# Kernel optimization log

Measured on AMD Instinct MI355X. Metric: run time of the kernel, lower is better.

Reference implementation:

```python
import jax, jax.numpy as jnp
import numpy as np
from jax.scipy.special import logsumexp

B, T, LD, HD, K = 64, 2048, 16, 64, 8
TEMP = 1.0  # annealing=False
LOG2PI = float(np.log(2.0 * np.pi))


def setup_inputs() -> dict:
    key = jax.random.key(0)
    ks = jax.random.split(key, 10)
    return {
        "z": jax.random.normal(ks[0], (B, T, LD), jnp.float32),
        "pi": jax.random.normal(ks[1], (K,), jnp.float32) * 0.5,
        "Q": jax.random.normal(ks[2], (K, K), jnp.float32) * 0.5,
        "init_mean": jax.random.normal(ks[3], (K, LD), jnp.float32),
        # torch init: rand(K,1,1) * eye(LD) * 5  (a scale factor per state)
        "init_cov": jax.random.uniform(ks[4], (K, 1, 1), jnp.float32) * 5.0 * jnp.eye(LD, dtype=jnp.float32)[None],
        "covs": jnp.tile(jnp.eye(LD, dtype=jnp.float32)[None], (K, 1, 1)) + 0.05 * jax.random.normal(ks[5], (K, LD, LD), jnp.float32),
        "W1": jax.random.normal(ks[6], (K, HD, LD), jnp.float32) / np.sqrt(LD),
        "b1": jnp.zeros((K, HD), jnp.float32),
        "W2": jax.random.normal(ks[7], (K, LD, HD), jnp.float32) / np.sqrt(HD),
        "b2": jnp.zeros((K, LD), jnp.float32),
    }


def _chol_terms(C):
    """Sigma = C C^T + 1e-6 I ; return (L^{-1}, 0.5*logdet) per state."""
    dim = C.shape[-1]
    Sigma = C @ jnp.swapaxes(C, -1, -2) + 1e-6 * jnp.eye(dim, dtype=C.dtype)
    L = jnp.linalg.cholesky(Sigma)  # [K,D,D]
    Linv = jax.vmap(lambda l: jax.scipy.linalg.solve_triangular(l, jnp.eye(dim, dtype=C.dtype), lower=True))(L)
    logdet_half = jnp.sum(jnp.log(jnp.diagonal(L, axis1=-2, axis2=-1)), -1)  # [K]
    return Linv, logdet_half


def _mvn_logp(diff, Linv, logdet_half):
    # diff [B,t,K,D], Linv [K,D,D] -> [B,t,K]
    y = jnp.einsum('kde,btke->btkd', Linv, diff)
    maha = jnp.sum(y * y, -1)
    d = diff.shape[-1]
    return -0.5 * maha - logdet_half - 0.5 * d * LOG2PI


def reference(z, pi, Q, init_mean, init_cov, covs, W1, b1, W2, b2):
    # ---- local evidence: log p(z_1|s_1), log p(z_t | z_{t-1}, s_t)  [B,T,K]
    Linv0, ld0 = _chol_terms(init_cov)
    le1 = _mvn_logp(z[:, :1, None, :] - init_mean, Linv0, ld0)  # [B,1,K]
    zp = z[:, :-1]  # [B,T-1,D]
    h = jax.nn.softplus(jnp.einsum('btd,khd->btkh', zp, W1) + b1)  # per-state MLP hidden
    mu = jnp.einsum('btkh,kdh->btkd', h, W2) + b2  # [B,T-1,K,D]
    LinvT, ldT = _chol_terms(covs)
    leT = _mvn_logp(z[:, 1:, None, :] - mu, LinvT, ldT)  # [B,T-1,K]
    le = jnp.concatenate([le1, leT], axis=1)  # [B,T,K]

    # ---- alpha recursion (filtering)
    logpi = jax.nn.log_softmax(pi / TEMP)
    Qlog = jax.nn.log_softmax(Q / TEMP, axis=-1)  # log p(s_t=j | s_{t-1}=i)
    QT = Qlog.T  # [to, from]
    lp0 = le[:, 0] + logpi
    lz0 = logsumexp(lp0, -1)
    la0 = lp0 - lz0[:, None]
    le_rest = jnp.swapaxes(le[:, 1:], 0, 1)  # [T-1,B,K]

    def astep(la_prev, le_t):
        lp = logsumexp(le_t[:, :, None] + QT[None] + la_prev[:, None, :], axis=-1)
        lz = logsumexp(lp, -1)
        la = lp - lz[:, None]
        return la, (la, lz)

    _, (las, lzs) = jax.lax.scan(astep, la0, le_rest)
    log_alpha = jnp.concatenate([la0[:, None], jnp.swapaxes(las, 0, 1)], axis=1)  # [B,T,K]
    log_Z = jnp.concatenate([lz0[:, None], lzs.T], axis=1)  # [B,T]

    # ---- beta recursion (smoothing), reverse scan
    def bstep(lb_next, inp):
        le_t, lz_t = inp
        lb = logsumexp(Qlog[None] + le_t[:, None, :] + lb_next[:, None, :], axis=-1) - lz_t[:, None]
        return lb, lb

    _, lbs = jax.lax.scan(bstep, jnp.zeros((B, K), le.dtype), (le_rest, log_Z[:, 1:].T), reverse=True)
    log_beta = jnp.concatenate([jnp.swapaxes(lbs, 0, 1), jnp.zeros((B, 1, K), le.dtype)], axis=1)

    # ---- posteriors
    gamma = jnp.exp(log_alpha + log_beta)  # [B,T,K]
    paired = jnp.exp(Qlog[None, None] + log_alpha[:, :-1, :, None] + log_beta[:, 1:, None, :] + le[:, 1:, None, :] - log_Z[:, 1:, None, None])  # [B,T-1,K,K]
    return gamma, paired, log_Z
```

## Files before the change

kernel.cpp:

```cpp
#include <hip/hip_runtime.h>

#define B_ 64
#define T_ 2048
#define LD_ 16
#define HD_ 64
#define K_ 8
#define L_ 16
#define C_ 128
#define S_ 16

constexpr int OFF_LE    = 0;
constexpr int OFF_ALPHA = 1048576;
constexpr int OFF_EBAR  = 2097152;
constexpr int OFF_ZT    = OFF_ALPHA;
constexpr int OFF_PBUF  = 3145728;
constexpr int OFF_RLOG  = 3670016;
constexpr int OFF_SBUF  = 3809280;
constexpr int OFF_UBUF  = 3874816;
constexpr int OFF_ULOG  = 3940352;
constexpr int OFF_SAIN  = 3941376;
constexpr int OFF_BENT  = 3949568;
constexpr int OFF_PRM   = 3957760;

constexpr int P_LINV0 = 0;
constexpr int P_LINVT = 2048;
constexpr int P_LD0   = 4096;
constexpr int P_LDT   = 4104;
constexpr int P_LOGPI = 4112;
constexpr int P_QEXP  = 4120;
constexpr int P_QTEXP = 4184;

constexpr int FI_NC2 = 32768;
constexpr int FI_C0I = 32896;

constexpr int OUT_PAIRED = B_*T_*K_;
constexpr int OUT_LOGZ   = OUT_PAIRED + B_*(T_-1)*K_*K_;

template<int CTRL>
__device__ __forceinline__ float dppmov(float x) {
  int xi = __float_as_int(x);
  int r = __builtin_amdgcn_update_dpp(xi, xi, CTRL, 0xF, 0xF, true);
  return __int_as_float(r);
}
__device__ __forceinline__ void allg8(float v, float w[8]) {
  w[0] = v;
  w[1] = dppmov<0xB1>(v);
  w[2] = dppmov<0x4E>(v);
  w[3] = dppmov<0x4E>(w[1]);
  w[7] = dppmov<0x141>(v);
  w[6] = dppmov<0xB1>(w[7]);
  w[5] = dppmov<0x4E>(w[7]);
  w[4] = dppmov<0x4E>(w[6]);
}
template<int V> __device__ __forceinline__ float xorg8(float x);
template<> __device__ __forceinline__ float xorg8<0>(float x) { return x; }
template<> __device__ __forceinline__ float xorg8<1>(float x) { return dppmov<0xB1>(x); }
template<> __device__ __forceinline__ float xorg8<2>(float x) { return dppmov<0x4E>(x); }
template<> __device__ __forceinline__ float xorg8<3>(float x) { return dppmov<0x4E>(dppmov<0xB1>(x)); }
template<> __device__ __forceinline__ float xorg8<4>(float x) { return dppmov<0x4E>(dppmov<0xB1>(dppmov<0x141>(x))); }
template<> __device__ __forceinline__ float xorg8<5>(float x) { return dppmov<0x4E>(dppmov<0x141>(x)); }
template<> __device__ __forceinline__ float xorg8<6>(float x) { return dppmov<0xB1>(dppmov<0x141>(x)); }
template<> __device__ __forceinline__ float xorg8<7>(float x) { return dppmov<0x141>(x); }

__device__ __forceinline__ float bfly_sum8(float x) {
  x += dppmov<0xB1>(x); x += dppmov<0x4E>(x); x += dppmov<0x141>(x); return x;
}
__device__ __forceinline__ float bfly_max8(float x) {
  x = fmaxf(x, dppmov<0xB1>(x)); x = fmaxf(x, dppmov<0x4E>(x)); x = fmaxf(x, dppmov<0x141>(x)); return x;
}
__device__ __forceinline__ float rcpnr(float x) {
  float r0 = __builtin_amdgcn_rcpf(x);
  return r0 * __builtin_fmaf(-x, r0, 2.0f);
}
__device__ __forceinline__ void absg8(float v, float w[8]) {
  int x = __float_as_int(v);
  w[0] = __int_as_float(__builtin_amdgcn_ds_swizzle(x, 0x18));
  w[1] = __int_as_float(__builtin_amdgcn_ds_swizzle(x, 0x38));
  w[2] = __int_as_float(__builtin_amdgcn_ds_swizzle(x, 0x58));
  w[3] = __int_as_float(__builtin_amdgcn_ds_swizzle(x, 0x78));
  w[4] = __int_as_float(__builtin_amdgcn_ds_swizzle(x, 0x98));
  w[5] = __int_as_float(__builtin_amdgcn_ds_swizzle(x, 0xB8));
  w[6] = __int_as_float(__builtin_amdgcn_ds_swizzle(x, 0xD8));
  w[7] = __int_as_float(__builtin_amdgcn_ds_swizzle(x, 0xF8));
}
__device__ __forceinline__ void col2row(const float cl[8], float rv[8]) {
  rv[0] = cl[0];
  rv[1] = xorg8<1>(cl[1]);
  rv[2] = xorg8<2>(cl[2]);
  rv[3] = xorg8<3>(cl[3]);
  rv[4] = xorg8<4>(cl[4]);
  rv[5] = xorg8<5>(cl[5]);
  rv[6] = xorg8<6>(cl[6]);
  rv[7] = xorg8<7>(cl[7]);
}
__device__ __forceinline__ void mmul8(const float a[8], const float m[8], float o[8]) {
  float m8[8][8];
  #pragma unroll
  for (int w = 0; w < 8; w++) allg8(m[w], m8[w]);
  #pragma unroll
  for (int v = 0; v < 8; v++) {
    float acc = 0.f;
    #pragma unroll
    for (int u = 0; u < 8; u++) acc = __builtin_fmaf(a[u], m8[u^v][u], acc);
    o[v] = acc;
  }
}
__device__ __forceinline__ float maxnorm8(float m[8]) {
  float mx = m[0];
  #pragma unroll
  for (int u = 1; u < 8; u++) mx = fmaxf(mx, m[u]);
  mx = bfly_max8(mx);
  float r = rcpnr(mx);
  #pragma unroll
  for (int u = 0; u < 8; u++) m[u] *= r;
  return mx;
}
__device__ __forceinline__ void load_rows(const float* p, float r[8]) {
  const float4* q = (const float4*)p;
  float4 x0 = q[0], x1 = q[1];
  r[0]=x0.x; r[1]=x0.y; r[2]=x0.z; r[3]=x0.w;
  r[4]=x1.x; r[5]=x1.y; r[6]=x1.z; r[7]=x1.w;
}
__device__ __forceinline__ float dotw8(const float r[8], const float w[8]) {
  return ((r[0]*w[0]+r[1]*w[1]) + (r[2]*w[2]+r[3]*w[3]))
       + ((r[4]*w[4]+r[5]*w[5]) + (r[6]*w[6]+r[7]*w[7]));
}

typedef __attribute__((ext_vector_type(4))) float f32x4;
typedef __attribute__((ext_vector_type(8))) short bf16x8;

__device__ __forceinline__ unsigned ph(float a, float b) {
  return (__float_as_uint(a) >> 16) | (__float_as_uint(b) & 0xFFFF0000u);
}
__device__ __forceinline__ float hif(float a) {
  return __uint_as_float(__float_as_uint(a) & 0xFFFF0000u);
}
__device__ __forceinline__ bf16x8 u2f(uint4 u) {
  return __builtin_bit_cast(bf16x8, u);
}
__device__ __forceinline__ bf16x8 mkfrag(float4 v) {
  unsigned ux = __float_as_uint(v.x), uy = __float_as_uint(v.y);
  unsigned uz = __float_as_uint(v.z), uw = __float_as_uint(v.w);
  unsigned h01 = (ux >> 16) | (uy & 0xFFFF0000u);
  unsigned h23 = (uz >> 16) | (uw & 0xFFFF0000u);
  float lx = v.x - __uint_as_float(ux & 0xFFFF0000u);
  float ly = v.y - __uint_as_float(uy & 0xFFFF0000u);
  float lz = v.z - __uint_as_float(uz & 0xFFFF0000u);
  float lw = v.w - __uint_as_float(uw & 0xFFFF0000u);
  unsigned l01 = ph(lx, ly);
  unsigned l23 = ph(lz, lw);
  return u2f(make_uint4(h01, h23, l01, l23));
}
__device__ __forceinline__ f32x4 MF(bf16x8 a, bf16x8 b, f32x4 c) {
  return __builtin_amdgcn_mfma_f32_16x16x32_bf16(a, b, c, 0, 0, 0);
}

__global__ __launch_bounds__(64) void prep_kernel(
    const float* __restrict__ pi, const float* __restrict__ Q,
    const float* __restrict__ init_cov, const float* __restrict__ covs,
    float* __restrict__ prm)
{
  int tid = threadIdx.x;
  int blk = blockIdx.x;
  if (blk < 16) {
    int k = blk & 7;
    const float* C = (blk < 8 ? init_cov : covs) + k*256;
    float* outL  = prm + (blk < 8 ? P_LINV0 : P_LINVT) + k*256;
    float* outld = prm + (blk < 8 ? P_LD0   : P_LDT)   + k;
    __shared__ float S[16][17], L[16][17], X[16][17];
    for (int e = tid; e < 256; e += 64) {
      int r = e >> 4, c = e & 15;
      float s = (r == c) ? 1e-6f : 0.f;
      for (int l = 0; l < 16; l++) s += C[r*16+l] * C[c*16+l];
      S[r][c] = s;
    }
    __syncthreads();
    for (int j = 0; j < 16; j++) {
      if (tid == 0) L[j][j] = sqrtf(S[j][j]);
      __syncthreads();
      if (tid > j && tid < 16) L[tid][j] = S[tid][j] / L[j][j];
      __syncthreads();
      if (tid > j && tid < 16) {
        float ltj = L[tid][j];
        for (int c = j+1; c <= tid; c++) S[tid][c] -= ltj * L[c][j];
      }
      __syncthreads();
    }
    if (tid < 16) {
      int c = tid;
      for (int r = 0; r < 16; r++) {
        float v;
        if (r < c) v = 0.f;
        else {
          v = (r == c) ? 1.f : 0.f;
          for (int s2 = c; s2 < r; s2++) v -= L[r][s2] * X[s2][c];
          v /= L[r][r];
        }
        X[r][c] = v;
      }
    }
    __syncthreads();
    for (int e = tid; e < 256; e += 64) outL[e] = X[e>>4][e&15];
    if (tid == 0) {
      float ld = 0.f;
      for (int j = 0; j < 16; j++) ld += logf(L[j][j]);
      *outld = ld;
    }
  } else {
    if (tid < 8) {
      int row = tid;
      float q[8], mx = -1e30f;
      for (int j = 0; j < 8; j++) { q[j] = Q[row*8+j]; mx = fmaxf(mx, q[j]); }
      float s = 0.f;
      for (int j = 0; j < 8; j++) s += __expf(q[j]-mx);
      float ls = logf(s);
      for (int j = 0; j < 8; j++) {
        float e = __expf(q[j]-mx-ls);
        prm[P_QEXP  + row*8 + j] = e;
        prm[P_QTEXP + j*8 + row] = e;
      }
    } else if (tid == 8) {
      float p[8], mx = -1e30f;
      for (int j = 0; j < 8; j++) { p[j] = pi[j]; mx = fmaxf(mx, p[j]); }
      float s = 0.f;
      for (int j = 0; j < 8; j++) s += __expf(p[j]-mx);
      float ls = logf(s);
      for (int j = 0; j < 8; j++) prm[P_LOGPI+j] = p[j]-mx-ls;
    }
  }
}

__global__ __launch_bounds__(64) void prep2_kernel(
    const float* __restrict__ W1, const float* __restrict__ W2,
    const float* __restrict__ b2, const float* __restrict__ init_mean,
    const float* __restrict__ prm, float* __restrict__ frag)
{
  int k = blockIdx.x, tid = threadIdx.x;
  __shared__ float Ls[16][16], L0s[16][16], G[16][64];
  for (int e = tid; e < 256; e += 64) {
    Ls[e>>4][e&15]  = prm[P_LINVT + k*256 + e];
    L0s[e>>4][e&15] = prm[P_LINV0 + k*256 + e];
  }
  __syncthreads();
  for (int idx = tid; idx < 1024; idx += 64) {
    int d = idx >> 6, hh = idx & 63;
    float s = 0.f;
    for (int e = 0; e < 16; e++) s += Ls[d][e] * W2[k*1024 + e*64 + hh];
    G[d][hh] = -s;
  }
  __syncthreads();
  int d = tid & 15, q = tid >> 4;
  uint4* F4 = (uint4*)frag;
  for (int kc = 0; kc < 2; kc++) {
    float v[8], lo[8];
    for (int j = 0; j < 8; j++) {
      int hh = 32*kc + 16*(j>>2) + 4*q + (j&3);
      v[j] = G[d][hh];
      lo[j] = v[j] - hif(v[j]);
    }
    F4[6144 + ((k*2+kc)*4+q)*16 + d] =
        make_uint4(ph(v[0],v[1]), ph(v[2],v[3]), ph(v[4],v[5]), ph(v[6],v[7]));
    F4[7168 + ((k*2+kc)*4+q)*16 + d] =
        make_uint4(ph(lo[0],lo[1]), ph(lo[2],lo[3]), ph(lo[4],lo[5]), ph(lo[6],lo[7]));
  }
  for (int mt = 0; mt < 4; mt++) {
    int hh = 16*mt + d;
    float v[4], lo[4];
    for (int j = 0; j < 4; j++) { v[j] = W1[k*1024 + hh*16 + 4*q + j]; lo[j] = v[j] - hif(v[j]); }
    unsigned x = ph(v[0],v[1]), y = ph(v[2],v[3]);
    F4[((k*4+mt)*4+q)*16 + d]        = make_uint4(x, y, x, y);
    F4[2048 + ((k*4+mt)*4+q)*16 + d] = make_uint4(ph(lo[0],lo[1]), ph(lo[2],lo[3]), 0u, 0u);
  }
  {
    float v[4], lo[4];
    for (int j = 0; j < 4; j++) { v[j] = Ls[d][4*q+j]; lo[j] = v[j] - hif(v[j]); }
    unsigned x = ph(v[0],v[1]), y = ph(v[2],v[3]);
    F4[4096 + (k*4+q)*16 + d] = make_uint4(x, y, x, y);
    F4[4608 + (k*4+q)*16 + d] = make_uint4(ph(lo[0],lo[1]), ph(lo[2],lo[3]), 0u, 0u);
    for (int j = 0; j < 4; j++) { v[j] = L0s[d][4*q+j]; lo[j] = v[j] - hif(v[j]); }
    x = ph(v[0],v[1]); y = ph(v[2],v[3]);
    F4[5120 + (k*4+q)*16 + d] = make_uint4(x, y, x, y);
    F4[5632 + (k*4+q)*16 + d] = make_uint4(ph(lo[0],lo[1]), ph(lo[2],lo[3]), 0u, 0u);
  }
  if (q == 0) {
    float s2 = 0.f, s0 = 0.f;
    for (int e = 0; e < 16; e++) {
      s2 += Ls[d][e]  * b2[k*16+e];
      s0 += L0s[d][e] * init_mean[k*16+e];
    }
    frag[FI_NC2 + k*16 + d] = -s2;
    frag[FI_C0I + k*16 + d] = -s0;
  }
}

__global__ __launch_bounds__(256) void ztr_kernel(
    const float* __restrict__ z, float* __restrict__ zt)
{
  int tid = blockIdx.x*256 + threadIdx.x;
  int t = tid >> 6, b = tid & 63;
  const float4* src = (const float4*)(z + (b*T_ + t)*LD_);
  float4* dst = (float4*)(zt + t*1024 + b*16);
  dst[0] = src[0]; dst[1] = src[1]; dst[2] = src[2]; dst[3] = src[3];
}

__global__ __launch_bounds__(256) void emisB_kernel(
    const float* __restrict__ zt, const float* __restrict__ b1,
    const float* __restrict__ frag, const float* __restrict__ prm,
    float* __restrict__ lebuf)
{
  int lane = threadIdx.x & 63;
  int wid = __builtin_amdgcn_readfirstlane(blockIdx.x*4 + (threadIdx.x >> 6));
  int bblk = wid & 3;
  int tch  = (wid >> 2) & 255;
  int k    = wid >> 10;
  int c = lane & 15, q = lane >> 4;
  int b = bblk*16 + c;
  const uint4* F4 = (const uint4*)frag;

  bf16x8 w1a1[4], w1a2[4];
  #pragma unroll
  for (int mt = 0; mt < 4; mt++) {
    w1a1[mt] = u2f(F4[((k*4+mt)*4+q)*16 + c]);
    w1a2[mt] = u2f(F4[2048 + ((k*4+mt)*4+q)*16 + c]);
  }
  bf16x8 lva1 = u2f(F4[4096 + (k*4+q)*16 + c]);
  bf16x8 lva2 = u2f(F4[4608 + (k*4+q)*16 + c]);
  bf16x8 gahi[2], galo[2];
  #pragma unroll
  for (int kc = 0; kc < 2; kc++) {
    gahi[kc] = u2f(F4[6144 + ((k*2+kc)*4+q)*16 + c]);
    galo[kc] = u2f(F4[7168 + ((k*2+kc)*4+q)*16 + c]);
  }
  float b1iv[16];
  #pragma unroll
  for (int i = 0; i < 16; i++)
    b1iv[i] = b1[k*64 + (i>>2)*16 + 4*q + (i&3)];
  float nc2[4];
  #pragma unroll
  for (int r = 0; r < 4; r++) nc2[r] = frag[FI_NC2 + k*16 + 4*q + r];
  float lconst = -prm[P_LDT + k] - 14.70301653f;

  int t0 = tch*8;
  bf16x8 zp;
  int ttstart;
  if (tch == 0) {
    float4 zv0 = *(const float4*)(zt + b*16 + 4*q);
    bf16x8 zc0 = mkfrag(zv0);
    bf16x8 l0a1 = u2f(F4[5120 + (k*4+q)*16 + c]);
    bf16x8 l0a2 = u2f(F4[5632 + (k*4+q)*16 + c]);
    f32x4 acc;
    acc[0] = frag[FI_C0I + k*16 + 4*q + 0];
    acc[1] = frag[FI_C0I + k*16 + 4*q + 1];
    acc[2] = frag[FI_C0I + k*16 + 4*q + 2];
    acc[3] = frag[FI_C0I + k*16 + 4*q + 3];
    acc = MF(l0a1, zc0, acc);
    acc = MF(l0a2, zc0, acc);
    float m2 = (acc[0]*acc[0] + acc[1]*acc[1]) + (acc[2]*acc[2] + acc[3]*acc[3]);
    m2 += __shfl_xor(m2, 16);
    m2 += __shfl_xor(m2, 32);
    float le = -0.5f*m2 - prm[P_LD0+k] - 14.70301653f + prm[P_LOGPI+k];
    if (q == 0) lebuf[k*64 + b] = le;
    zp = zc0;
    ttstart = 1;
  } else {
    float4 zvp = *(const float4*)(zt + (t0-1)*1024 + b*16 + 4*q);
    zp = mkfrag(zvp);
    ttstart = 0;
  }

  float4 zv = *(const float4*)(zt + (t0+ttstart)*1024 + b*16 + 4*q);
  #pragma unroll 1
  for (int tt = ttstart; tt < 8; tt++) {
    int t = t0 + tt;
    float4 zvn = zv;
    if (tt < 7) zvn = *(const float4*)(zt + (t+1)*1024 + b*16 + 4*q);
    bf16x8 zc = mkfrag(zv);
    f32x4 a1[4];
    #pragma unroll
    for (int mt = 0; mt < 4; mt++) {
      f32x4 ai;
      ai[0] = b1iv[mt*4+0]; ai[1] = b1iv[mt*4+1];
      ai[2] = b1iv[mt*4+2]; ai[3] = b1iv[mt*4+3];
      ai = MF(w1a1[mt], zp, ai);
      a1[mt] = MF(w1a2[mt], zp, ai);
    }
    float hv[16];
    #pragma unroll
    for (int i = 0; i < 16; i++) {
      float a = a1[i>>2][i&3];
      hv[i] = fmaxf(a, 0.f) + __logf(1.f + __expf(-fabsf(a)));
    }
    bf16x8 hhi[2], hlo[2];
    #pragma unroll
    for (int kc = 0; kc < 2; kc++) {
      const float* hp = hv + 8*kc;
      hhi[kc] = u2f(make_uint4(ph(hp[0],hp[1]), ph(hp[2],hp[3]),
                               ph(hp[4],hp[5]), ph(hp[6],hp[7])));
      float l0 = hp[0]-hif(hp[0]), l1 = hp[1]-hif(hp[1]);
      float l2 = hp[2]-hif(hp[2]), l3 = hp[3]-hif(hp[3]);
      float l4 = hp[4]-hif(hp[4]), l5 = hp[5]-hif(hp[5]);
      float l6 = hp[6]-hif(hp[6]), l7 = hp[7]-hif(hp[7]);
      hlo[kc] = u2f(make_uint4(ph(l0,l1), ph(l2,l3), ph(l4,l5), ph(l6,l7)));
    }
    f32x4 acc;
    acc[0] = nc2[0]; acc[1] = nc2[1]; acc[2] = nc2[2]; acc[3] = nc2[3];
    acc = MF(lva1, zc, acc);
    acc = MF(lva2, zc, acc);
    #pragma unroll
    for (int kc = 0; kc < 2; kc++) {
      acc = MF(gahi[kc], hhi[kc], acc);
      acc = MF(galo[kc], hhi[kc], acc);
      acc = MF(gahi[kc], hlo[kc], acc);
    }
    float m2 = (acc[0]*acc[0] + acc[1]*acc[1]) + (acc[2]*acc[2] + acc[3]*acc[3]);
    m2 += __shfl_xor(m2, 16);
    m2 += __shfl_xor(m2, 32);
    float le = -0.5f*m2 + lconst;
    if (q == 0) lebuf[t*512 + k*64 + b] = le;
    zp = zc;
    zv = zvn;
  }
}

__global__ __launch_bounds__(256) void fwdA_kernel(
    const float* __restrict__ lebuf, const float* __restrict__ prm,
    float* __restrict__ pbuf, float* __restrict__ sbuf)
{
  int lane64 = threadIdx.x & 63;
  int iu = threadIdx.x >> 6;
  int unit = blockIdx.x*4 + iu;
  int b = unit & 63, s = unit >> 6;
  int u = lane64 >> 3, j = lane64 & 7;
  int c = 8*s + u;
  float qtv[64];
  #pragma unroll
  for (int x = 0; x < 8; x++)
    #pragma unroll
    for (int v = 0; v < 8; v++)
      qtv[x*8+v] = prm[P_QTEXP + (j^x)*8 + (j^v)];
  float lev[16];
  #pragma unroll
  for (int x = 0; x < 16; x++) lev[x] = lebuf[(c*L_+x)*512 + j*64 + b];
  float pl[8];
  if (c == 0) {
    float m = bfly_max8(lev[0]);
    float e = __expf(lev[0]-m);
    allg8(e, pl);
  } else {
    float m = bfly_max8(lev[0]);
    float e = __expf(lev[0]-m);
    float e8[8]; allg8(e, e8);
    float np[8];
    #pragma unroll
    for (int x = 0; x < 8; x++) np[x] = e8[x] * qtv[x*8];
    float mx = np[0];
    #pragma unroll
    for (int x = 1; x < 8; x++) mx = fmaxf(mx, np[x]);
    mx = bfly_max8(mx);
    float r = rcpnr(mx);
    #pragma unroll
    for (int x = 0; x < 8; x++) pl[x] = np[x] * r;
  }
  #pragma unroll
  for (int sx = 1; sx < 16; sx++) {
    float m = bfly_max8(lev[sx]);
    float e = __expf(lev[sx]-m);
    float e8[8]; allg8(e, e8);
    float np[8];
    #pragma unroll
    for (int x = 0; x < 8; x++) {
      float acc = 0.f;
      #pragma unroll
      for (int v = 0; v < 8; v++) acc = __builtin_fmaf(qtv[x*8+v], pl[v], acc);
      np[x] = e8[x] * acc;
    }
    float mx = np[0];
    #pragma unroll
    for (int x = 1; x < 8; x++) mx = fmaxf(mx, np[x]);
    mx = bfly_max8(mx);
    float r = rcpnr(mx);
    #pragma unroll
    for (int x = 0; x < 8; x++) pl[x] = np[x] * r;
  }
  float rv[8]; col2row(pl, rv);
  float4* dst = (float4*)(pbuf + (c*64 + b)*64 + j*8);
  dst[0] = make_float4(rv[0], rv[1], rv[2], rv[3]);
  dst[1] = make_float4(rv[4], rv[5], rv[6], rv[7]);
  __shared__ float M[4][8][64];
  #pragma unroll
  for (int v = 0; v < 8; v++) M[iu][u][j*8+v] = rv[v];
  __syncthreads();
  if (u == 0) {
    float m[8];
    #pragma unroll
    for (int v = 0; v < 8; v++) m[v] = M[iu][0][j*8+v];
    for (int cc = 1; cc < 8; cc++) {
      float a[8];
      #pragma unroll
      for (int v = 0; v < 8; v++) a[v] = M[iu][cc][j*8+v];
      float nm[8];
      mmul8(a, m, nm);
      maxnorm8(nm);
      #pragma unroll
      for (int v = 0; v < 8; v++) m[v] = nm[v];
    }
    float4* d2 = (float4*)(sbuf + (s*64 + b)*64 + j*8);
    d2[0] = make_float4(m[0], m[1], m[2], m[3]);
    d2[1] = make_float4(m[4], m[5], m[6], m[7]);
  }
}

__global__ __launch_bounds__(512) void fwdP2b_kernel(
    const float* __restrict__ sbuf, float* __restrict__ sain)
{
  int lane = threadIdx.x;
  int b = lane >> 3, i = lane & 7;
  const float4* base = (const float4*)sbuf;
  float4 c0 = base[(0*64+b)*16 + i*2], c1 = base[(0*64+b)*16 + i*2 + 1];
  float a = 0.125f;
  for (int s = 0; s < 16; s++) {
    int s2 = (s < 15) ? s+1 : 15;
    float4 n0 = base[(s2*64+b)*16 + i*2], n1 = base[(s2*64+b)*16 + i*2 + 1];
    float aw[8]; allg8(a, aw);
    float sm = ((c0.x*aw[0] + c0.y*aw[1]) + (c0.z*aw[2] + c0.w*aw[3]))
             + ((c1.x*aw[4] + c1.y*aw[5]) + (c1.z*aw[6] + c1.w*aw[7]));
    float tot = bfly_sum8(sm);
    float an = sm * rcpnr(tot);
    if (s < 15) { a = an; sain[(s+1)*512 + b*8 + i] = a; }
    c0 = n0; c1 = n1;
  }
}

__global__ __launch_bounds__(256) void fwdB_kernel(
    const float* __restrict__ lebuf, const float* __restrict__ prm,
    const float* __restrict__ sain, float* pbuf,
    float* __restrict__ alpha, float* __restrict__ ebar,
    float* __restrict__ rlog, float* __restrict__ ubuf,
    float* __restrict__ ulog, float* __restrict__ out)
{
  int lane64 = threadIdx.x & 63;
  int iu = threadIdx.x >> 6;
  int unit = blockIdx.x*4 + iu;
  int b = unit & 63, s = unit >> 6;
  int u = lane64 >> 3, i = lane64 & 7;
  int c = 8*s + u;
  int off = b*8 + i;
  __shared__ float Als[4][8];
  __shared__ float Mh[4][8][64];
  __shared__ float Lh[4][8];
  float pr[8];
  load_rows(pbuf + (c*64 + b)*64 + i*8, pr);
  float lev[16];
  #pragma unroll
  for (int x = 0; x < 16; x++) lev[x] = lebuf[(c*L_+x)*512 + i*64 + b];
  float av_in = 0.f;
  if (u == 0) av_in = (s == 0) ? 0.125f : sain[s*512 + off];
  for (int r = 0; r < 7; r++) {
    if (u == r) {
      if (r > 0) av_in = Als[iu][i];
      float aw[8]; allg8(av_in, aw);
      float sm = dotw8(pr, aw);
      float tot = bfly_sum8(sm);
      Als[iu][i] = sm * rcpnr(tot);
    }
    __syncthreads();
  }
  if (u == 7) av_in = Als[iu][i];
  float q[8];
  #pragma unroll
  for (int x = 0; x < 8; x++) q[x] = prm[P_QTEXP + i*8 + (i^x)];
  float* logZ = out + OUT_LOGZ + b*T_;
  float eb_loc[16];
  float a;
  if (c == 0) {
    float m0 = bfly_max8(lev[0]);
    float e0x = __expf(lev[0]-m0);
    float ct = bfly_sum8(e0x);
    float rr = rcpnr(ct);
    a = e0x * rr;
    alpha[off] = a;
    eb_loc[0] = a;
    ebar[off] = a;
    if (i == 0) logZ[0] = m0 + __logf(ct);
  } else {
    a = av_in;
    int t = c*L_;
    float m = bfly_max8(lev[0]);
    float e = __expf(lev[0]-m);
    float w[8]; allg8(a, w);
    float dot = dotw8(q, w);
    float p = e * dot;
    float ct = bfly_sum8(p);
    float rr = rcpnr(ct);
    a = p * rr;
    alpha[t*512 + off] = a;
    float eb = e * rr;
    eb_loc[0] = eb;
    ebar[t*512 + off] = eb;
    if (i == 0) logZ[t] = m + __logf(ct);
  }
  #pragma unroll
  for (int x = 1; x < 16; x++) {
    int t = c*L_ + x;
    float m = bfly_max8(lev[x]);
    float e = __expf(lev[x]-m);
    float w[8]; allg8(a, w);
    float dot = dotw8(q, w);
    float p = e * dot;
    float ct = bfly_sum8(p);
    float rr = rcpnr(ct);
    a = p * rr;
    alpha[t*512 + off] = a;
    float eb = e * rr;
    eb_loc[x] = eb;
    ebar[t*512 + off] = eb;
    if (i == 0) logZ[t] = m + __logf(ct);
  }
  float qv[64];
  #pragma unroll
  for (int x = 0; x < 8; x++)
    #pragma unroll
    for (int v = 0; v < 8; v++)
      qv[x*8+v] = prm[P_QEXP + (i^x)*8 + (i^v)];
  float rl8[8];
  #pragma unroll
  for (int x = 0; x < 8; x++) rl8[x] = (x == 0) ? 1.f : 0.f;
  float lsc = 0.f;
  #pragma unroll
  for (int sx = 15; sx >= 1; sx--) {
    float e8[8]; allg8(eb_loc[sx], e8);
    float nr[8];
    #pragma unroll
    for (int x = 0; x < 8; x++) {
      float acc = 0.f;
      #pragma unroll
      for (int v = 0; v < 8; v++) acc = __builtin_fmaf(qv[x*8+v], e8[v]*rl8[v], acc);
      nr[x] = acc;
    }
    float mx = nr[0];
    #pragma unroll
    for (int x = 1; x < 8; x++) mx = fmaxf(mx, nr[x]);
    mx = bfly_max8(mx);
    float r = rcpnr(mx);
    #pragma unroll
    for (int x = 0; x < 8; x++) rl8[x] = nr[x] * r;
    lsc += __logf(mx);
  }
  float rv[8]; col2row(rl8, rv);
  float4* dstR = (float4*)(pbuf + (c*64 + b)*64 + i*8);
  dstR[0] = make_float4(rv[0], rv[1], rv[2], rv[3]);
  dstR[1] = make_float4(rv[4], rv[5], rv[6], rv[7]);
  if (i == 0) rlog[c*64 + b] = lsc;
  float qr[8];
  #pragma unroll
  for (int x = 0; x < 8; x++) qr[x] = prm[P_QEXP + i*8 + (i^x)];
  float d8[8];
  #pragma unroll
  for (int v = 0; v < 8; v++) d8[v] = eb_loc[0] * rv[v];
  float h8[8];
  mmul8(qr, d8, h8);
  float ls = lsc + __logf(maxnorm8(h8));
  #pragma unroll
  for (int v = 0; v < 8; v++) Mh[iu][u][i*8+v] = h8[v];
  if (i == 0) Lh[iu][u] = ls;
  __syncthreads();
  if (u == 0) {
    float m[8];
    #pragma unroll
    for (int v = 0; v < 8; v++) m[v] = Mh[iu][7][i*8+v];
    float lsum = Lh[iu][7];
    for (int cc = 6; cc >= 0; cc--) {
      float aa[8];
      #pragma unroll
      for (int v = 0; v < 8; v++) aa[v] = Mh[iu][cc][i*8+v];
      float t8[8];
      mmul8(aa, m, t8);
      lsum += Lh[iu][cc] + __logf(maxnorm8(t8));
      #pragma unroll
      for (int v = 0; v < 8; v++) m[v] = t8[v];
    }
    float4* d2 = (float4*)(ubuf + (s*64 + b)*64 + i*8);
    d2[0] = make_float4(m[0], m[1], m[2], m[3]);
    d2[1] = make_float4(m[4], m[5], m[6], m[7]);
    if (i == 0) ulog[s*64 + b] = lsum;
  }
}

__global__ __launch_bounds__(512) void bwdP2b_kernel(
    const float* __restrict__ ubuf, const float* __restrict__ ulog,
    float* __restrict__ bent)
{
  int lane = threadIdx.x;
  int b = lane >> 3, i = lane & 7;
  bent[15*512 + b*8 + i] = 1.f;
  const float4* base = (const float4*)ubuf;
  float sh = 1.f, sig = 0.f;
  float4 c0 = base[(15*64+b)*16 + i*2], c1 = base[(15*64+b)*16 + i*2 + 1];
  float cu = ulog[15*64 + b];
  for (int s = 15; s >= 1; s--) {
    int s2 = (s > 1) ? s-1 : 1;
    float4 n0 = base[(s2*64+b)*16 + i*2], n1 = base[(s2*64+b)*16 + i*2 + 1];
    float nu = ulog[s2*64 + b];
    float sw[8]; allg8(sh, sw);
    float y = ((c0.x*sw[0] + c0.y*sw[1]) + (c0.z*sw[2] + c0.w*sw[3]))
            + ((c1.x*sw[4] + c1.y*sw[5]) + (c1.z*sw[6] + c1.w*sw[7]));
    float mx = bfly_max8(y);
    sh = y * rcpnr(mx);
    sig += cu + __logf(mx);
    bent[(s-1)*512 + b*8 + i] = sh * __expf(sig);
    c0 = n0; c1 = n1; cu = nu;
  }
}

__global__ __launch_bounds__(256) void bwdC_kernel(
    const float* __restrict__ alpha, const float* __restrict__ ebar,
    const float* __restrict__ rbuf, const float* __restrict__ rlog,
    const float* __restrict__ prm, const float* __restrict__ bent,
    float* __restrict__ out)
{
  int lane64 = threadIdx.x & 63;
  int iu = threadIdx.x >> 6;
  int unit = blockIdx.x*4 + iu;
  int b = unit & 63, s = unit >> 6;
  int u = lane64 >> 3, i = lane64 & 7;
  int c = 8*s + u;
  int off = b*8 + i;
  float qr[8], qa[8];
  #pragma unroll
  for (int x = 0; x < 8; x++) qr[x] = prm[P_QEXP + i*8 + (i^x)];
  #pragma unroll
  for (int v = 0; v < 8; v++) qa[v] = prm[P_QEXP + i*8 + v];
  float r8[8];
  load_rows(rbuf + (c*64 + b)*64 + i*8, r8);
  float e0 = ebar[(c*L_)*512 + off];
  float erl = __expf(rlog[c*64 + b]);
  float av[16], ev[16];
  #pragma unroll
  for (int x = 0; x < 16; x++) av[x] = alpha[(c*L_+x)*512 + off];
  #pragma unroll
  for (int x = 1; x < 16; x++) ev[x] = ebar[(c*L_+x)*512 + off];
  float avm1 = (c > 0) ? alpha[(c*L_-1)*512 + off] : 0.f;
  __shared__ float Bls[4][8];
  float bt = 0.f, y = 0.f, nbv = 0.f;
  for (int r = 7; r >= 0; r--) {
    if (u == r) {
      bt = (r == 7) ? bent[s*512 + off] : Bls[iu][i];
      float bw[8]; allg8(bt, bw);
      y = dotw8(r8, bw) * erl;
      float ey = e0 * y;
      float w[8]; allg8(ey, w);
      nbv = 0.f;
      #pragma unroll
      for (int v = 0; v < 8; v++) nbv = __builtin_fmaf(qr[v], w[v], nbv);
      if (r > 0) Bls[iu][i] = nbv;
    }
    __syncthreads();
  }
  float* po = out + OUT_PAIRED + b*((T_-1)*64);
  float* go = out + b*(T_*K_);
  float bb = bt;
  if (c == 127) go[2047*8 + i] = av[15];
  #pragma unroll
  for (int x = 15; x >= 1; x--) {
    float eya[8]; absg8(ev[x]*bb, eya);
    float term[8];
    #pragma unroll
    for (int v = 0; v < 8; v++) term[v] = qa[v]*eya[v];
    float nb = ((term[0]+term[1]) + (term[2]+term[3]))
             + ((term[4]+term[5]) + (term[6]+term[7]));
    int t = c*L_ + x - 1;
    float am = av[x-1];
    float4* pd = (float4*)(po + t*64 + i*8);
    pd[0] = make_float4(am*term[0], am*term[1], am*term[2], am*term[3]);
    pd[1] = make_float4(am*term[4], am*term[5], am*term[6], am*term[7]);
    go[t*8 + i] = am*nb;
    bb = nb;
  }
  if (c > 0) {
    float eya[8]; absg8(e0*y, eya);
    int t = c*L_ - 1;
    float4* pd = (float4*)(po + t*64 + i*8);
    pd[0] = make_float4(avm1*qa[0]*eya[0], avm1*qa[1]*eya[1],
                        avm1*qa[2]*eya[2], avm1*qa[3]*eya[3]);
    pd[1] = make_float4(avm1*qa[4]*eya[4], avm1*qa[5]*eya[5],
                        avm1*qa[6]*eya[6], avm1*qa[7]*eya[7]);
    go[t*8 + i] = avm1 * nbv;
  }
}

extern "C" void kernel_launch(void* const* d_in, const int* in_sizes, int n_in,
                              void* d_out, int out_size, void* d_ws, size_t ws_size,
                              hipStream_t stream) {
  const float* z         = (const float*)d_in[0];
  const float* pi        = (const float*)d_in[1];
  const float* Q         = (const float*)d_in[2];
  const float* init_mean = (const float*)d_in[3];
  const float* init_cov  = (const float*)d_in[4];
  const float* covs      = (const float*)d_in[5];
  const float* W1        = (const float*)d_in[6];
  const float* b1        = (const float*)d_in[7];
  const float* W2        = (const float*)d_in[8];
  const float* b2        = (const float*)d_in[9];
  float* out = (float*)d_out;
  float* ws  = (float*)d_ws;

  prep_kernel<<<17, 64, 0, stream>>>(pi, Q, init_cov, covs, ws + OFF_PRM);
  prep2_kernel<<<8, 64, 0, stream>>>(W1, W2, b2, init_mean, ws + OFF_PRM,
                                     ws + OFF_UBUF);
  ztr_kernel<<<512, 256, 0, stream>>>(z, ws + OFF_ZT);
  emisB_kernel<<<2048, 256, 0, stream>>>(ws + OFF_ZT, b1, ws + OFF_UBUF,
                                         ws + OFF_PRM, ws + OFF_LE);
  fwdA_kernel<<<256, 256, 0, stream>>>(ws + OFF_LE, ws + OFF_PRM,
                                       ws + OFF_PBUF, ws + OFF_SBUF);
  fwdP2b_kernel<<<1, 512, 0, stream>>>(ws + OFF_SBUF, ws + OFF_SAIN);
  fwdB_kernel<<<256, 256, 0, stream>>>(ws + OFF_LE, ws + OFF_PRM, ws + OFF_SAIN,
                                       ws + OFF_PBUF, ws + OFF_ALPHA,
                                       ws + OFF_EBAR, ws + OFF_RLOG,
                                       ws + OFF_UBUF, ws + OFF_ULOG, out);
  bwdP2b_kernel<<<1, 512, 0, stream>>>(ws + OFF_UBUF, ws + OFF_ULOG, ws + OFF_BENT);
  bwdC_kernel<<<256, 256, 0, stream>>>(ws + OFF_ALPHA, ws + OFF_EBAR,
                                       ws + OFF_PBUF, ws + OFF_RLOG,
                                       ws + OFF_PRM, ws + OFF_BENT, out);
}
```

Measured before the change: 230.8 us.

## Repack le/alpha/ebar buffers chunk-major and precompute bf16 z fragments and Q permutations

Changes the layout of the emission, alpha and ebar workspace buffers so each (chunk, batch, state) owns 16 contiguous time steps, letting the forward and backward kernels use vectorized float4 loads and stores instead of strided scalar accesses. The transpose kernel now emits precomputed hi/lo bf16 MFMA fragments of z, so the emission kernel no longer splits them itself. The XOR-permuted Q tables are precomputed once in prep2 for vector loads. Softplus is simplified to log(1+exp(a)), which can overflow for large activations, and the t=0 emission write in the new layout depends on correct indexing.

```diff
diff --git a/kernel.cpp b/kernel.cpp
--- a/kernel.cpp
+++ b/kernel.cpp
@@ -29,6 +29,8 @@
 constexpr int P_LOGPI = 4112;
 constexpr int P_QEXP  = 4120;
 constexpr int P_QTEXP = 4184;
+constexpr int P_QTV   = 4256;
+constexpr int P_QV    = 4768;
 
 constexpr int FI_NC2 = 32768;
 constexpr int FI_C0I = 32896;
@@ -121,6 +123,21 @@
   r[0]=x0.x; r[1]=x0.y; r[2]=x0.z; r[3]=x0.w;
   r[4]=x1.x; r[5]=x1.y; r[6]=x1.z; r[7]=x1.w;
 }
+__device__ __forceinline__ void load16(const float* p, float r[16]) {
+  const float4* q = (const float4*)p;
+  float4 a0=q[0], a1=q[1], a2=q[2], a3=q[3];
+  r[0]=a0.x; r[1]=a0.y; r[2]=a0.z; r[3]=a0.w;
+  r[4]=a1.x; r[5]=a1.y; r[6]=a1.z; r[7]=a1.w;
+  r[8]=a2.x; r[9]=a2.y; r[10]=a2.z; r[11]=a2.w;
+  r[12]=a3.x; r[13]=a3.y; r[14]=a3.z; r[15]=a3.w;
+}
+__device__ __forceinline__ void store16(float* p, const float r[16]) {
+  float4* q = (float4*)p;
+  q[0] = make_float4(r[0],r[1],r[2],r[3]);
+  q[1] = make_float4(r[4],r[5],r[6],r[7]);
+  q[2] = make_float4(r[8],r[9],r[10],r[11]);
+  q[3] = make_float4(r[12],r[13],r[14],r[15]);
+}
 __device__ __forceinline__ float dotw8(const float r[8], const float w[8]) {
   return ((r[0]*w[0]+r[1]*w[1]) + (r[2]*w[2]+r[3]*w[3]))
        + ((r[4]*w[4]+r[5]*w[5]) + (r[6]*w[6]+r[7]*w[7]));
@@ -138,7 +155,7 @@
 __device__ __forceinline__ bf16x8 u2f(uint4 u) {
   return __builtin_bit_cast(bf16x8, u);
 }
-__device__ __forceinline__ bf16x8 mkfrag(float4 v) {
+__device__ __forceinline__ uint4 mkfrag_u4(float4 v) {
   unsigned ux = __float_as_uint(v.x), uy = __float_as_uint(v.y);
   unsigned uz = __float_as_uint(v.z), uw = __float_as_uint(v.w);
   unsigned h01 = (ux >> 16) | (uy & 0xFFFF0000u);
@@ -149,7 +166,7 @@
   float lw = v.w - __uint_as_float(uw & 0xFFFF0000u);
   unsigned l01 = ph(lx, ly);
   unsigned l23 = ph(lz, lw);
-  return u2f(make_uint4(h01, h23, l01, l23));
+  return make_uint4(h01, h23, l01, l23);
 }
 __device__ __forceinline__ f32x4 MF(bf16x8 a, bf16x8 b, f32x4 c) {
   return __builtin_amdgcn_mfma_f32_16x16x32_bf16(a, b, c, 0, 0, 0);
@@ -233,9 +250,16 @@
 __global__ __launch_bounds__(64) void prep2_kernel(
     const float* __restrict__ W1, const float* __restrict__ W2,
     const float* __restrict__ b2, const float* __restrict__ init_mean,
-    const float* __restrict__ prm, float* __restrict__ frag)
+    float* __restrict__ prm, float* __restrict__ frag)
 {
   int k = blockIdx.x, tid = threadIdx.x;
+  if (k == 0) {
+    int j = tid >> 3, x = tid & 7;
+    for (int v = 0; v < 8; v++) {
+      prm[P_QTV + j*64 + x*8 + v] = prm[P_QTEXP + (j^x)*8 + (j^v)];
+      prm[P_QV  + j*64 + x*8 + v] = prm[P_QEXP  + (j^x)*8 + (j^v)];
+    }
+  }
   __shared__ float Ls[16][16], L0s[16][16], G[16][64];
   for (int e = tid; e < 256; e += 64) {
     Ls[e>>4][e&15]  = prm[P_LINVT + k*256 + e];
@@ -294,17 +318,18 @@
 }
 
 __global__ __launch_bounds__(256) void ztr_kernel(
-    const float* __restrict__ z, float* __restrict__ zt)
+    const float* __restrict__ z, uint4* __restrict__ zf)
 {
   int tid = blockIdx.x*256 + threadIdx.x;
   int t = tid >> 6, b = tid & 63;
   const float4* src = (const float4*)(z + (b*T_ + t)*LD_);
-  float4* dst = (float4*)(zt + t*1024 + b*16);
-  dst[0] = src[0]; dst[1] = src[1]; dst[2] = src[2]; dst[3] = src[3];
+  #pragma unroll
+  for (int q = 0; q < 4; q++)
+    zf[(t*4 + q)*64 + b] = mkfrag_u4(src[q]);
 }
 
 __global__ __launch_bounds__(256) void emisB_kernel(
-    const float* __restrict__ zt, const float* __restrict__ b1,
+    const uint4* __restrict__ zf, const float* __restrict__ b1,
     const float* __restrict__ frag, const float* __restrict__ prm,
     float* __restrict__ lebuf)
 {
@@ -344,8 +369,7 @@
   bf16x8 zp;
   int ttstart;
   if (tch == 0) {
-    float4 zv0 = *(const float4*)(zt + b*16 + 4*q);
-    bf16x8 zc0 = mkfrag(zv0);
+    bf16x8 zc0 = u2f(zf[q*64 + b]);
     bf16x8 l0a1 = u2f(F4[5120 + (k*4+q)*16 + c]);
     bf16x8 l0a2 = u2f(F4[5632 + (k*4+q)*16 + c]);
     f32x4 acc;
@@ -359,22 +383,21 @@
     m2 += __shfl_xor(m2, 16);
     m2 += __shfl_xor(m2, 32);
     float le = -0.5f*m2 - prm[P_LD0+k] - 14.70301653f + prm[P_LOGPI+k];
-    if (q == 0) lebuf[k*64 + b] = le;
+    if (q == 0) lebuf[(b*8 + k)*16] = le;
     zp = zc0;
     ttstart = 1;
   } else {
-    float4 zvp = *(const float4*)(zt + (t0-1)*1024 + b*16 + 4*q);
-    zp = mkfrag(zvp);
+    zp = u2f(zf[((t0-1)*4 + q)*64 + b]);
     ttstart = 0;
   }
 
-  float4 zv = *(const float4*)(zt + (t0+ttstart)*1024 + b*16 + 4*q);
+  uint4 zvu = zf[((t0+ttstart)*4 + q)*64 + b];
   #pragma unroll 1
   for (int tt = ttstart; tt < 8; tt++) {
     int t = t0 + tt;
-    float4 zvn = zv;
-    if (tt < 7) zvn = *(const float4*)(zt + (t+1)*1024 + b*16 + 4*q);
-    bf16x8 zc = mkfrag(zv);
+    uint4 zvn = zvu;
+    if (tt < 7) zvn = zf[((t+1)*4 + q)*64 + b];
+    bf16x8 zc = u2f(zvu);
     f32x4 a1[4];
     #pragma unroll
     for (int mt = 0; mt < 4; mt++) {
@@ -388,7 +411,7 @@
     #pragma unroll
     for (int i = 0; i < 16; i++) {
       float a = a1[i>>2][i&3];
-      hv[i] = fmaxf(a, 0.f) + __logf(1.f + __expf(-fabsf(a)));
+      hv[i] = __logf(1.f + __expf(a));
     }
     bf16x8 hhi[2], hlo[2];
     #pragma unroll
@@ -416,9 +439,9 @@
     m2 += __shfl_xor(m2, 16);
     m2 += __shfl_xor(m2, 32);
     float le = -0.5f*m2 + lconst;
-    if (q == 0) lebuf[t*512 + k*64 + b] = le;
+    if (q == 0) lebuf[(((t>>4)*64 + b)*8 + k)*16 + (t&15)] = le;
     zp = zc;
-    zv = zvn;
+    zvu = zvn;
   }
 }
 
@@ -433,14 +456,12 @@
   int u = lane64 >> 3, j = lane64 & 7;
   int c = 8*s + u;
   float qtv[64];
-  #pragma unroll
-  for (int x = 0; x < 8; x++)
-    #pragma unroll
-    for (int v = 0; v < 8; v++)
-      qtv[x*8+v] = prm[P_QTEXP + (j^x)*8 + (j^v)];
+  load16(prm + P_QTV + j*64,      qtv);
+  load16(prm + P_QTV + j*64 + 16, qtv+16);
+  load16(prm + P_QTV + j*64 + 32, qtv+32);
+  load16(prm + P_QTV + j*64 + 48, qtv+48);
   float lev[16];
-  #pragma unroll
-  for (int x = 0; x < 16; x++) lev[x] = lebuf[(c*L_+x)*512 + j*64 + b];
+  load16(lebuf + ((c*64 + b)*8 + j)*16, lev);
   float pl[8];
   if (c == 0) {
     float m = bfly_max8(lev[0]);
@@ -551,8 +572,7 @@
   float pr[8];
   load_rows(pbuf + (c*64 + b)*64 + i*8, pr);
   float lev[16];
-  #pragma unroll
-  for (int x = 0; x < 16; x++) lev[x] = lebuf[(c*L_+x)*512 + i*64 + b];
+  load16(lebuf + ((c*64 + b)*8 + i)*16, lev);
   float av_in = 0.f;
   if (u == 0) av_in = (s == 0) ? 0.125f : sain[s*512 + off];
   for (int r = 0; r < 7; r++) {
@@ -570,7 +590,7 @@
   #pragma unroll
   for (int x = 0; x < 8; x++) q[x] = prm[P_QTEXP + i*8 + (i^x)];
   float* logZ = out + OUT_LOGZ + b*T_;
-  float eb_loc[16];
+  float av_arr[16], eb_loc[16];
   float a;
   if (c == 0) {
     float m0 = bfly_max8(lev[0]);
@@ -578,13 +598,11 @@
     float ct = bfly_sum8(e0x);
     float rr = rcpnr(ct);
     a = e0x * rr;
-    alpha[off] = a;
+    av_arr[0] = a;
     eb_loc[0] = a;
-    ebar[off] = a;
     if (i == 0) logZ[0] = m0 + __logf(ct);
   } else {
     a = av_in;
-    int t = c*L_;
     float m = bfly_max8(lev[0]);
     float e = __expf(lev[0]-m);
     float w[8]; allg8(a, w);
@@ -593,15 +611,12 @@
     float ct = bfly_sum8(p);
     float rr = rcpnr(ct);
     a = p * rr;
-    alpha[t*512 + off] = a;
-    float eb = e * rr;
-    eb_loc[0] = eb;
-    ebar[t*512 + off] = eb;
-    if (i == 0) logZ[t] = m + __logf(ct);
+    av_arr[0] = a;
+    eb_loc[0] = e * rr;
+    if (i == 0) logZ[c*L_] = m + __logf(ct);
   }
   #pragma unroll
   for (int x = 1; x < 16; x++) {
-    int t = c*L_ + x;
     float m = bfly_max8(lev[x]);
     float e = __expf(lev[x]-m);
     float w[8]; allg8(a, w);
@@ -610,18 +625,17 @@
     float ct = bfly_sum8(p);
     float rr = rcpnr(ct);
     a = p * rr;
-    alpha[t*512 + off] = a;
-    float eb = e * rr;
-    eb_loc[x] = eb;
-    ebar[t*512 + off] = eb;
-    if (i == 0) logZ[t] = m + __logf(ct);
-  }
+    av_arr[x] = a;
+    eb_loc[x] = e * rr;
+    if (i == 0) logZ[c*L_ + x] = m + __logf(ct);
+  }
+  store16(alpha + ((c*64 + b)*8 + i)*16, av_arr);
+  store16(ebar  + ((c*64 + b)*8 + i)*16, eb_loc);
   float qv[64];
-  #pragma unroll
-  for (int x = 0; x < 8; x++)
-    #pragma unroll
-    for (int v = 0; v < 8; v++)
-      qv[x*8+v] = prm[P_QEXP + (i^x)*8 + (i^v)];
+  load16(prm + P_QV + i*64,      qv);
+  load16(prm + P_QV + i*64 + 16, qv+16);
+  load16(prm + P_QV + i*64 + 32, qv+32);
+  load16(prm + P_QV + i*64 + 48, qv+48);
   float rl8[8];
   #pragma unroll
   for (int x = 0; x < 8; x++) rl8[x] = (x == 0) ? 1.f : 0.f;
@@ -732,14 +746,13 @@
   for (int v = 0; v < 8; v++) qa[v] = prm[P_QEXP + i*8 + v];
   float r8[8];
   load_rows(rbuf + (c*64 + b)*64 + i*8, r8);
-  float e0 = ebar[(c*L_)*512 + off];
   float erl = __expf(rlog[c*64 + b]);
+  int base = ((c*64 + b)*8 + i)*16;
   float av[16], ev[16];
-  #pragma unroll
-  for (int x = 0; x < 16; x++) av[x] = alpha[(c*L_+x)*512 + off];
-  #pragma unroll
-  for (int x = 1; x < 16; x++) ev[x] = ebar[(c*L_+x)*512 + off];
-  float avm1 = (c > 0) ? alpha[(c*L_-1)*512 + off] : 0.f;
+  load16(alpha + base, av);
+  load16(ebar  + base, ev);
+  float e0 = ev[0];
+  float avm1 = (c > 0) ? alpha[base - 8192 + 15] : 0.f;
   __shared__ float Bls[4][8];
   float bt = 0.f, y = 0.f, nbv = 0.f;
   for (int r = 7; r >= 0; r--) {
@@ -807,9 +820,10 @@
   prep_kernel<<<17, 64, 0, stream>>>(pi, Q, init_cov, covs, ws + OFF_PRM);
   prep2_kernel<<<8, 64, 0, stream>>>(W1, W2, b2, init_mean, ws + OFF_PRM,
                                      ws + OFF_UBUF);
-  ztr_kernel<<<512, 256, 0, stream>>>(z, ws + OFF_ZT);
-  emisB_kernel<<<2048, 256, 0, stream>>>(ws + OFF_ZT, b1, ws + OFF_UBUF,
-                                         ws + OFF_PRM, ws + OFF_LE);
+  ztr_kernel<<<512, 256, 0, stream>>>(z, (uint4*)(ws + OFF_ZT));
+  emisB_kernel<<<2048, 256, 0, stream>>>((const uint4*)(ws + OFF_ZT), b1,
+                                         ws + OFF_UBUF, ws + OFF_PRM,
+                                         ws + OFF_LE);
   fwdA_kernel<<<256, 256, 0, stream>>>(ws + OFF_LE, ws + OFF_PRM,
                                        ws + OFF_PBUF, ws + OFF_SBUF);
   fwdP2b_kernel<<<1, 512, 0, stream>>>(ws + OFF_SBUF, ws + OFF_SAIN);
```

Result: slower. 264.4 us (+14.6%).
